# Kernel optimization log

Measured on AMD Instinct MI355X. Metric: run time of the kernel, lower is better.

## Reference

```python
import jax, jax.numpy as jnp
import numpy as np

B, N_COLS, N_PROMPTS, D = 1024, 256, 128, 256


def _ln(x, g, b, eps=1e-5):
    m = jnp.mean(x, axis=-1, keepdims=True)
    v = jnp.mean(jnp.square(x - m), axis=-1, keepdims=True)
    return (x - m) * jax.lax.rsqrt(v + eps) * g + b


def setup_inputs() -> dict:
    key = jax.random.key(0)
    ks = jax.random.split(key, 10)
    d_rs = D ** -0.5
    return {
        "x": jax.random.normal(ks[0], (B, N_COLS), jnp.float32),
        "prev_cell_out": jax.random.normal(ks[1], (B, N_PROMPTS, D), jnp.float32),
        "feature_emb_weight": jax.random.uniform(ks[2], (N_COLS, D), jnp.float32, -d_rs, d_rs),
        "feature_emb_bias": jax.random.uniform(ks[3], (N_COLS, D), jnp.float32, -d_rs, d_rs),
        "ln_emb_g": jnp.ones((D,), jnp.float32),
        "ln_emb_b": jnp.zeros((D,), jnp.float32),
        "ln_col_g": jnp.ones((D,), jnp.float32),
        "ln_col_b": jnp.zeros((D,), jnp.float32),
        "ln_prompt_g": jnp.ones((D,), jnp.float32),
        "ln_prompt_b": jnp.zeros((D,), jnp.float32),
        # torch Linear(2*D, D): weight [D, 2*D], y = x @ W^T + b
        "dense_imp_w": jax.random.normal(ks[4], (D, 2 * D), jnp.float32) * (2 * D) ** -0.5,
        "dense_imp_b": jnp.zeros((D,), jnp.float32),
        "emb_column": jax.random.normal(ks[5], (N_COLS, D), jnp.float32) * 0.01,
        "emb_prompt": jax.random.normal(ks[6], (N_PROMPTS, D), jnp.float32) * 0.01,
        # dense_expand = Linear(1, n_prompts): weight [n_prompts,1] squeezed -> [n_prompts]
        "expand_w": jax.random.normal(ks[7], (N_PROMPTS,), jnp.float32),
        "expand_b": jax.random.normal(ks[8], (N_PROMPTS,), jnp.float32) * 0.01,
    }


def reference(x, prev_cell_out, feature_emb_weight, feature_emb_bias,
              ln_emb_g, ln_emb_b, ln_col_g, ln_col_b, ln_prompt_g, ln_prompt_b,
              dense_imp_w, dense_imp_b, emb_column, emb_prompt,
              expand_w, expand_b):
    # feature embedding: [B, N, D]
    x_emb = jax.nn.relu(jnp.einsum('bn,nd->bnd', x, feature_emb_weight) + feature_emb_bias)
    x_emb = _ln(x_emb, ln_emb_g, ln_emb_b)
    # prompt update with residual
    xp = jnp.broadcast_to(emb_prompt[None], (x.shape[0], N_PROMPTS, D))  # [B, P, D]
    cat = jnp.concatenate([_ln(xp, ln_prompt_g, ln_prompt_b), prev_cell_out], axis=-1)  # [B, P, 2D]
    xp = jnp.einsum('bpk,dk->bpd', cat, dense_imp_w) + dense_imp_b + xp
    # column keys (shared across batch)
    col = _ln(emb_column, ln_col_g, ln_col_b)  # [N, D]
    mask = jax.nn.softmax(jnp.einsum('bpd,nd->bpn', xp, col), axis=-1)  # [B, P, N]
    V = jnp.einsum('bpn,bnd->bpd', mask, x_emb)  # [B, P, D]
    return V * (1.0 + expand_w)[None, :, None] + expand_b[None, :, None]
```

## Files before the change

kernel.cpp:

```cpp
#include <hip/hip_runtime.h>

#define NCOLS 256
#define NP    128
#define DD    256

typedef _Float16 half2 __attribute__((ext_vector_type(2)));
typedef _Float16 half4 __attribute__((ext_vector_type(4)));
typedef _Float16 half8 __attribute__((ext_vector_type(8)));
typedef float    f32x4 __attribute__((ext_vector_type(4)));

#define MFMA16(a,b,c) __builtin_amdgcn_mfma_f32_16x16x16f16(a,b,c,0,0,0)
#define MFMA32(a,b,c) __builtin_amdgcn_mfma_f32_16x16x32_f16(a,b,c,0,0,0)

#define WS_COL_LN   0
#define WS_BASE     393216
#define WS_BLOG     524288
#define WS_CW16     655360
#define WS_WB16     786432

#define LDS_CWP   3072
#define LDS_XE0   68608
#define LDS_XE1   101376
#define SMEM_MAIN 134144

__global__ __launch_bounds__(256) void k_prep1(
    const float* __restrict__ emb_column, const float* __restrict__ emb_prompt,
    const float* __restrict__ ln_col_g, const float* __restrict__ ln_col_b,
    const float* __restrict__ ln_prompt_g, const float* __restrict__ ln_prompt_b,
    const float* __restrict__ few, const float* __restrict__ feb,
    const float* __restrict__ diw, const float* __restrict__ dib,
    char* __restrict__ ws)
{
    __shared__ float red[10];
    __shared__ float rowv[DD];
    int blk = blockIdx.x, tid = threadIdx.x;

    if (blk < 384) {
        bool isCol = blk < 256;
        int r = isCol ? blk : blk - 256;
        const float* src = (isCol ? emb_column : emb_prompt) + r*DD;
        const float* g   = isCol ? ln_col_g : ln_prompt_g;
        const float* bb  = isCol ? ln_col_b : ln_prompt_b;

        float v = src[tid];
        float s = v, q = v*v;
        #pragma unroll
        for (int off = 32; off; off >>= 1) { s += __shfl_xor(s, off); q += __shfl_xor(q, off); }
        int wid = tid >> 6, lane = tid & 63;
        if (lane == 0) { red[wid] = s; red[4+wid] = q; }
        __syncthreads();
        if (tid == 0) {
            float S = red[0]+red[1]+red[2]+red[3];
            float Q = red[4]+red[5]+red[6]+red[7];
            float mu = S * (1.0f/DD);
            float var = Q * (1.0f/DD) - mu*mu;
            red[8] = mu; red[9] = rsqrtf(var + 1e-5f);
        }
        __syncthreads();
        float ln = (v - red[8]) * red[9] * g[tid] + bb[tid];
        rowv[tid] = ln;
        if (isCol) ((float*)(ws + WS_COL_LN))[r*DD + tid] = ln;
        __syncthreads();

        if (isCol) {
            int n = r;
            float acc = 0.f;
            #pragma unroll 4
            for (int d = 0; d < DD; ++d) acc += rowv[d] * diw[d*512 + 256 + tid];
            int nt = n >> 4, lr = n & 15;
            int kc32 = tid >> 5, lq = (tid >> 3) & 3, jj = tid & 7;
            ((_Float16*)(ws + WS_CW16))[(kc32*16 + nt)*512 + (lq*16 + lr)*8 + jj] = (_Float16)acc;
        } else {
            int p = r;
            float acc = 0.f;
            #pragma unroll 4
            for (int k = 0; k < DD; ++k) acc += rowv[k] * diw[tid*512 + k];
            ((float*)(ws + WS_BASE))[p*DD + tid] = acc + dib[tid] + emb_prompt[p*DD + tid];
        }
    } else {
        int base = (blk - 384) * 512;
        half2* wb = (half2*)(ws + WS_WB16);
        #pragma unroll
        for (int j = 0; j < 2; ++j) {
            int idx = base + j*256 + tid;
            half2 h; h[0] = (_Float16)few[idx]; h[1] = (_Float16)feb[idx];
            wb[idx] = h;
        }
    }
}

__global__ __launch_bounds__(256) void k_prep2(char* __restrict__ ws)
{
    __shared__ float bs[DD];
    int p = blockIdx.x, n = threadIdx.x;
    const float* base   = (const float*)(ws + WS_BASE);
    const float* col_ln = (const float*)(ws + WS_COL_LN);
    bs[n] = base[p*DD + n];
    __syncthreads();
    float acc = 0.f;
    #pragma unroll 4
    for (int d = 0; d < DD; ++d) acc += bs[d] * col_ln[n*DD + d];
    ((float*)(ws + WS_BLOG))[p*DD + n] = acc;
}

__global__ __launch_bounds__(1024) void trompt_main(
    const float* __restrict__ x, const float* __restrict__ prev,
    const float* __restrict__ expand_w, const float* __restrict__ expand_b,
    const float* __restrict__ ln_emb_g, const float* __restrict__ ln_emb_b,
    const char* __restrict__ ws, float* __restrict__ out)
{
    extern __shared__ char smem[];
    float* x_s  = (float*)(smem);
    float* sm_m = (float*)(smem + 1024);
    float* sm_l = (float*)(smem + 2048);
    char*  cwP  = smem + LDS_CWP;
    char*  xe0  = smem + LDS_XE0;
    char*  xe1  = smem + LDS_XE1;

    const char*  cwbase = ws + WS_CW16;
    const half2* WB     = (const half2*)(ws + WS_WB16);

    int b = blockIdx.x;
    int tid = threadIdx.x;
    int w = tid >> 6, l = tid & 63, lq = l >> 4, lr = l & 15;
    int pt = w >> 1, h = w & 1;
    int p  = 16*pt + lr;
    int pswz = (p & 7) << 4;

    if (tid < 256) x_s[tid] = x[b*NCOLS + tid];

    half8 pf[8];
    {
        const float* prow = prev + ((size_t)b*NP + p)*DD + 8*lq;
        #pragma unroll
        for (int kc = 0; kc < 8; ++kc) {
            f32x4 v0 = *(const f32x4*)(prow + 32*kc);
            f32x4 v1 = *(const f32x4*)(prow + 32*kc + 4);
            half8 hh;
            #pragma unroll
            for (int j = 0; j < 4; ++j) { hh[j] = (_Float16)v0[j]; hh[4+j] = (_Float16)v1[j]; }
            pf[kc] = hh;
        }
    }

    f32x4 acc[8];
    {
        const float* blrow = (const float*)(ws + WS_BLOG) + (size_t)p*DD + 4*lq;
        #pragma unroll
        for (int a = 0; a < 8; ++a) acc[a] = *(const f32x4*)(blrow + 16*(8*h + a));
    }

    #pragma unroll
    for (int i = 0; i < 8; ++i) {
        int u = tid + 1024*i;
        *(uint4*)(cwP + u*16) = *(const uint4*)(cwbase + u*16);
    }

    __syncthreads();

    {
        const char* cwl = cwP + (size_t)(8*h)*1024 + l*16;
        #pragma unroll
        for (int kc = 0; kc < 8; ++kc) {
            const char* fb = cwl + (size_t)kc*16384;
            half8 bp = pf[kc];
            #pragma unroll
            for (int a = 0; a < 8; ++a)
                acc[a] = MFMA32(*(const half8*)(fb + a*1024), bp, acc[a]);
        }
    }

    float mh = -1e30f;
    #pragma unroll
    for (int a = 0; a < 8; ++a)
        #pragma unroll
        for (int r = 0; r < 4; ++r) mh = fmaxf(mh, acc[a][r]);
    mh = fmaxf(mh, __shfl_xor(mh, 16));
    mh = fmaxf(mh, __shfl_xor(mh, 32));

    float sh = 0.f;
    #pragma unroll
    for (int a = 0; a < 8; ++a)
        #pragma unroll
        for (int r = 0; r < 4; ++r) { float e = __expf(acc[a][r] - mh); acc[a][r] = e; sh += e; }
    sh += __shfl_xor(sh, 16);
    sh += __shfl_xor(sh, 32);

    if (lq == 0) { sm_m[h*128 + p] = mh; sm_l[h*128 + p] = sh; }
    __syncthreads();
    float mo = sm_m[(1 ^ h)*128 + p];
    float so = sm_l[(1 ^ h)*128 + p];
    float M  = fmaxf(mh, mo);
    float eh = __expf(mh - M), eo = __expf(mo - M);
    float fac = eh / (sh*eh + so*eo);

    #pragma unroll
    for (int a = 0; a < 8; ++a) {
        int nb = (8*h + a)*32 + lq*8;
        half4 hh;
        #pragma unroll
        for (int r = 0; r < 4; ++r) hh[r] = (_Float16)(acc[a][r] * fac);
        *(half4*)(cwP + p*512 + (nb ^ pswz)) = hh;
    }

    float gcc[4], bcc[4];
    #pragma unroll
    for (int cc = 0; cc < 4; ++cc) {
        gcc[cc] = ln_emb_g[l + 64*cc];
        bcc[cc] = ln_emb_b[l + 64*cc];
    }

    int kc2w = w >> 2, lq2 = w & 3;
    auto compute_xe = [&](int c, char* xebuf) {
        float vj[4][4];
        #pragma unroll
        for (int j = 0; j < 4; ++j) {
            int n = c*64 + 16*kc2w + 4*lq2 + j;
            float xv = x_s[n];
            const half2* wbrow = WB + n*DD;
            float ss = 0.f, qq = 0.f;
            #pragma unroll
            for (int cc = 0; cc < 4; ++cc) {
                half2 pp = wbrow[l + 64*cc];
                float e = fmaf(xv, (float)pp[0], (float)pp[1]);
                e = e > 0.f ? e : 0.f;
                vj[j][cc] = e; ss += e; qq += e*e;
            }
            #pragma unroll
            for (int off = 32; off; off >>= 1) { ss += __shfl_xor(ss, off); qq += __shfl_xor(qq, off); }
            float mu = ss * (1.0f/DD);
            float rs = rsqrtf(qq*(1.0f/DD) - mu*mu + 1e-5f);
            #pragma unroll
            for (int cc = 0; cc < 4; ++cc)
                vj[j][cc] = (vj[j][cc]-mu)*rs*gcc[cc] + bcc[cc];
        }
        #pragma unroll
        for (int cc = 0; cc < 4; ++cc) {
            int dt = 4*cc + (l >> 4);
            half4 hh;
            #pragma unroll
            for (int j = 0; j < 4; ++j) hh[j] = (_Float16)vj[j][cc];
            *(half4*)(xebuf + (((kc2w*16 + dt)*64) + lq2*16 + lr)*8) = hh;
        }
    };

    compute_xe(0, xe0);

    f32x4 acc_v[8];
    #pragma unroll
    for (int dtl = 0; dtl < 8; ++dtl) acc_v[dtl] = (f32x4){0.f,0.f,0.f,0.f};

    __syncthreads();

    for (int c = 0; c < 4; ++c) {
        char* xec = (c & 1) ? xe1 : xe0;
        char* xen = (c & 1) ? xe0 : xe1;

        half4 bp[4];
        #pragma unroll
        for (int kc2 = 0; kc2 < 4; ++kc2)
            bp[kc2] = *(const half4*)(cwP + p*512 + ((c*128 + kc2*32 + lq*8) ^ pswz));

        if (c < 3) compute_xe(c+1, xen);

        const char* xel = xec + l*8;
        #pragma unroll
        for (int kc2 = 0; kc2 < 4; ++kc2) {
            const char* xb = xel + (size_t)(kc2*16 + 8*h)*512;
            half4 bpc = bp[kc2];
            #pragma unroll
            for (int dtl = 0; dtl < 8; ++dtl)
                acc_v[dtl] = MFMA16(*(const half4*)(xb + dtl*512), bpc, acc_v[dtl]);
        }

        if (c < 3) __syncthreads();
    }

    {
        float sw = 1.0f + expand_w[p];
        float sb = expand_b[p];
        float* orow = out + ((size_t)b*NP + p)*DD + 128*h + 4*lq;
        #pragma unroll
        for (int dtl = 0; dtl < 8; ++dtl) {
            f32x4 v = acc_v[dtl];
            #pragma unroll
            for (int r = 0; r < 4; ++r) v[r] = v[r]*sw + sb;
            *(f32x4*)(orow + 16*dtl) = v;
        }
    }
}

extern "C" void kernel_launch(void* const* d_in, const int* in_sizes, int n_in,
                              void* d_out, int out_size, void* d_ws, size_t ws_size,
                              hipStream_t stream) {
    (void)in_sizes; (void)n_in; (void)out_size; (void)ws_size;
    const float* x           = (const float*)d_in[0];
    const float* prev        = (const float*)d_in[1];
    const float* few         = (const float*)d_in[2];
    const float* feb         = (const float*)d_in[3];
    const float* ln_emb_g    = (const float*)d_in[4];
    const float* ln_emb_b    = (const float*)d_in[5];
    const float* ln_col_g    = (const float*)d_in[6];
    const float* ln_col_b    = (const float*)d_in[7];
    const float* ln_prompt_g = (const float*)d_in[8];
    const float* ln_prompt_b = (const float*)d_in[9];
    const float* diw         = (const float*)d_in[10];
    const float* dib         = (const float*)d_in[11];
    const float* emb_column  = (const float*)d_in[12];
    const float* emb_prompt  = (const float*)d_in[13];
    const float* expand_w    = (const float*)d_in[14];
    const float* expand_b    = (const float*)d_in[15];
    char* ws = (char*)d_ws;
    float* out = (float*)d_out;

    k_prep1<<<512, 256, 0, stream>>>(emb_column, emb_prompt, ln_col_g, ln_col_b,
                                     ln_prompt_g, ln_prompt_b, few, feb,
                                     diw, dib, ws);
    k_prep2<<<128, 256, 0, stream>>>(ws);

    (void)hipFuncSetAttribute(reinterpret_cast<const void*>(trompt_main),
                              hipFuncAttributeMaxDynamicSharedMemorySize, SMEM_MAIN);
    trompt_main<<<1024, 1024, SMEM_MAIN, stream>>>(x, prev, expand_w, expand_b,
                                                   ln_emb_g, ln_emb_b, ws, out);
}
```

Before: 181.3 us.

## Make main kernel persistent over four batches with prefetch of next batch inputs

The main kernel now launches 256 blocks, and each block loops over four batch rows instead of handling one. While the softmax and value stages of the current row run, it prefetches the next row's prev_cell_out fragment into registers and its x row into a second LDS buffer. The aim is to hide global load latency and amortise block launch and setup, since the LN gains and bias pointers are loaded once per block. In exchange there is less parallelism (256 blocks on a 256-CU part), more live registers from holding the prefetched fragment, and the column-weight tile is reloaded into LDS every iteration because its space is reused for the mask.

```diff
diff --git a/kernel.cpp b/kernel.cpp
--- a/kernel.cpp
+++ b/kernel.cpp
@@ -18,10 +18,10 @@
 #define WS_CW16     655360
 #define WS_WB16     786432
 
-#define LDS_CWP   3072
-#define LDS_XE0   68608
-#define LDS_XE1   101376
-#define SMEM_MAIN 134144
+#define LDS_CWP   4096
+#define LDS_XE0   69632
+#define LDS_XE1   102400
+#define SMEM_MAIN 135168
 
 __global__ __launch_bounds__(256) void k_prep1(
     const float* __restrict__ emb_column, const float* __restrict__ emb_prompt,
@@ -110,9 +110,10 @@
     const char* __restrict__ ws, float* __restrict__ out)
 {
     extern __shared__ char smem[];
-    float* x_s  = (float*)(smem);
-    float* sm_m = (float*)(smem + 1024);
-    float* sm_l = (float*)(smem + 2048);
+    float* x_sA = (float*)(smem);
+    float* x_sB = (float*)(smem + 1024);
+    float* sm_m = (float*)(smem + 2048);
+    float* sm_l = (float*)(smem + 3072);
     char*  cwP  = smem + LDS_CWP;
     char*  xe0  = smem + LDS_XE0;
     char*  xe1  = smem + LDS_XE1;
@@ -120,88 +121,13 @@
     const char*  cwbase = ws + WS_CW16;
     const half2* WB     = (const half2*)(ws + WS_WB16);
 
-    int b = blockIdx.x;
+    int bid = blockIdx.x;
     int tid = threadIdx.x;
     int w = tid >> 6, l = tid & 63, lq = l >> 4, lr = l & 15;
     int pt = w >> 1, h = w & 1;
     int p  = 16*pt + lr;
     int pswz = (p & 7) << 4;
-
-    if (tid < 256) x_s[tid] = x[b*NCOLS + tid];
-
-    half8 pf[8];
-    {
-        const float* prow = prev + ((size_t)b*NP + p)*DD + 8*lq;
-        #pragma unroll
-        for (int kc = 0; kc < 8; ++kc) {
-            f32x4 v0 = *(const f32x4*)(prow + 32*kc);
-            f32x4 v1 = *(const f32x4*)(prow + 32*kc + 4);
-            half8 hh;
-            #pragma unroll
-            for (int j = 0; j < 4; ++j) { hh[j] = (_Float16)v0[j]; hh[4+j] = (_Float16)v1[j]; }
-            pf[kc] = hh;
-        }
-    }
-
-    f32x4 acc[8];
-    {
-        const float* blrow = (const float*)(ws + WS_BLOG) + (size_t)p*DD + 4*lq;
-        #pragma unroll
-        for (int a = 0; a < 8; ++a) acc[a] = *(const f32x4*)(blrow + 16*(8*h + a));
-    }
-
-    #pragma unroll
-    for (int i = 0; i < 8; ++i) {
-        int u = tid + 1024*i;
-        *(uint4*)(cwP + u*16) = *(const uint4*)(cwbase + u*16);
-    }
-
-    __syncthreads();
-
-    {
-        const char* cwl = cwP + (size_t)(8*h)*1024 + l*16;
-        #pragma unroll
-        for (int kc = 0; kc < 8; ++kc) {
-            const char* fb = cwl + (size_t)kc*16384;
-            half8 bp = pf[kc];
-            #pragma unroll
-            for (int a = 0; a < 8; ++a)
-                acc[a] = MFMA32(*(const half8*)(fb + a*1024), bp, acc[a]);
-        }
-    }
-
-    float mh = -1e30f;
-    #pragma unroll
-    for (int a = 0; a < 8; ++a)
-        #pragma unroll
-        for (int r = 0; r < 4; ++r) mh = fmaxf(mh, acc[a][r]);
-    mh = fmaxf(mh, __shfl_xor(mh, 16));
-    mh = fmaxf(mh, __shfl_xor(mh, 32));
-
-    float sh = 0.f;
-    #pragma unroll
-    for (int a = 0; a < 8; ++a)
-        #pragma unroll
-        for (int r = 0; r < 4; ++r) { float e = __expf(acc[a][r] - mh); acc[a][r] = e; sh += e; }
-    sh += __shfl_xor(sh, 16);
-    sh += __shfl_xor(sh, 32);
-
-    if (lq == 0) { sm_m[h*128 + p] = mh; sm_l[h*128 + p] = sh; }
-    __syncthreads();
-    float mo = sm_m[(1 ^ h)*128 + p];
-    float so = sm_l[(1 ^ h)*128 + p];
-    float M  = fmaxf(mh, mo);
-    float eh = __expf(mh - M), eo = __expf(mo - M);
-    float fac = eh / (sh*eh + so*eo);
-
-    #pragma unroll
-    for (int a = 0; a < 8; ++a) {
-        int nb = (8*h + a)*32 + lq*8;
-        half4 hh;
-        #pragma unroll
-        for (int r = 0; r < 4; ++r) hh[r] = (_Float16)(acc[a][r] * fac);
-        *(half4*)(cwP + p*512 + (nb ^ pswz)) = hh;
-    }
+    int kc2w = w >> 2, lq2 = w & 3;
 
     float gcc[4], bcc[4];
     #pragma unroll
@@ -209,14 +135,28 @@
         gcc[cc] = ln_emb_g[l + 64*cc];
         bcc[cc] = ln_emb_b[l + 64*cc];
     }
-
-    int kc2w = w >> 2, lq2 = w & 3;
-    auto compute_xe = [&](int c, char* xebuf) {
+    const float* blrow = (const float*)(ws + WS_BLOG) + (size_t)p*DD + 4*lq;
+
+    half8 pf[8];
+    auto load_pf = [&](int bb) {
+        const float* prow = prev + ((size_t)bb*NP + p)*DD + 8*lq;
+        #pragma unroll
+        for (int kc = 0; kc < 8; ++kc) {
+            f32x4 v0 = *(const f32x4*)(prow + 32*kc);
+            f32x4 v1 = *(const f32x4*)(prow + 32*kc + 4);
+            half8 hh;
+            #pragma unroll
+            for (int j = 0; j < 4; ++j) { hh[j] = (_Float16)v0[j]; hh[4+j] = (_Float16)v1[j]; }
+            pf[kc] = hh;
+        }
+    };
+
+    auto compute_xe = [&](const float* xs, int c, char* xebuf) {
         float vj[4][4];
         #pragma unroll
         for (int j = 0; j < 4; ++j) {
             int n = c*64 + 16*kc2w + 4*lq2 + j;
-            float xv = x_s[n];
+            float xv = xs[n];
             const half2* wbrow = WB + n*DD;
             float ss = 0.f, qq = 0.f;
             #pragma unroll
@@ -244,48 +184,122 @@
         }
     };
 
-    compute_xe(0, xe0);
-
-    f32x4 acc_v[8];
-    #pragma unroll
-    for (int dtl = 0; dtl < 8; ++dtl) acc_v[dtl] = (f32x4){0.f,0.f,0.f,0.f};
-
-    __syncthreads();
-
-    for (int c = 0; c < 4; ++c) {
-        char* xec = (c & 1) ? xe1 : xe0;
-        char* xen = (c & 1) ? xe0 : xe1;
-
-        half4 bp[4];
-        #pragma unroll
-        for (int kc2 = 0; kc2 < 4; ++kc2)
-            bp[kc2] = *(const half4*)(cwP + p*512 + ((c*128 + kc2*32 + lq*8) ^ pswz));
-
-        if (c < 3) compute_xe(c+1, xen);
-
-        const char* xel = xec + l*8;
-        #pragma unroll
-        for (int kc2 = 0; kc2 < 4; ++kc2) {
-            const char* xb = xel + (size_t)(kc2*16 + 8*h)*512;
-            half4 bpc = bp[kc2];
-            #pragma unroll
-            for (int dtl = 0; dtl < 8; ++dtl)
-                acc_v[dtl] = MFMA16(*(const half4*)(xb + dtl*512), bpc, acc_v[dtl]);
-        }
-
-        if (c < 3) __syncthreads();
-    }
-
-    {
-        float sw = 1.0f + expand_w[p];
-        float sb = expand_b[p];
-        float* orow = out + ((size_t)b*NP + p)*DD + 128*h + 4*lq;
-        #pragma unroll
-        for (int dtl = 0; dtl < 8; ++dtl) {
-            f32x4 v = acc_v[dtl];
-            #pragma unroll
-            for (int r = 0; r < 4; ++r) v[r] = v[r]*sw + sb;
-            *(f32x4*)(orow + 16*dtl) = v;
+    if (tid < 256) x_sA[tid] = x[bid*NCOLS + tid];
+    load_pf(bid);
+
+    #pragma unroll 1
+    for (int it = 0; it < 4; ++it) {
+        int b = bid + 256*it;
+        const float* xs  = (it & 1) ? x_sB : x_sA;
+        float*       xsn = (it & 1) ? x_sA : x_sB;
+
+        __syncthreads();
+
+        #pragma unroll
+        for (int i = 0; i < 8; ++i) {
+            int u = tid + 1024*i;
+            *(uint4*)(cwP + u*16) = *(const uint4*)(cwbase + u*16);
+        }
+
+        f32x4 acc[8];
+        #pragma unroll
+        for (int a = 0; a < 8; ++a) acc[a] = *(const f32x4*)(blrow + 16*(8*h + a));
+
+        __syncthreads();
+
+        {
+            const char* cwl = cwP + (size_t)(8*h)*1024 + l*16;
+            #pragma unroll
+            for (int kc = 0; kc < 8; ++kc) {
+                const char* fb = cwl + (size_t)kc*16384;
+                half8 bp = pf[kc];
+                #pragma unroll
+                for (int a = 0; a < 8; ++a)
+                    acc[a] = MFMA32(*(const half8*)(fb + a*1024), bp, acc[a]);
+            }
+        }
+
+        if (it < 3) {
+            load_pf(b + 256);
+            if (tid < 256) xsn[tid] = x[(b + 256)*NCOLS + tid];
+        }
+
+        float mh = -1e30f;
+        #pragma unroll
+        for (int a = 0; a < 8; ++a)
+            #pragma unroll
+            for (int r = 0; r < 4; ++r) mh = fmaxf(mh, acc[a][r]);
+        mh = fmaxf(mh, __shfl_xor(mh, 16));
+        mh = fmaxf(mh, __shfl_xor(mh, 32));
+
+        float sh = 0.f;
+        #pragma unroll
+        for (int a = 0; a < 8; ++a)
+            #pragma unroll
+            for (int r = 0; r < 4; ++r) { float e = __expf(acc[a][r] - mh); acc[a][r] = e; sh += e; }
+        sh += __shfl_xor(sh, 16);
+        sh += __shfl_xor(sh, 32);
+
+        if (lq == 0) { sm_m[h*128 + p] = mh; sm_l[h*128 + p] = sh; }
+        __syncthreads();
+        float mo = sm_m[(1 ^ h)*128 + p];
+        float so = sm_l[(1 ^ h)*128 + p];
+        float M  = fmaxf(mh, mo);
+        float eh = __expf(mh - M), eo = __expf(mo - M);
+        float fac = eh / (sh*eh + so*eo);
+
+        #pragma unroll
+        for (int a = 0; a < 8; ++a) {
+            int nb = (8*h + a)*32 + lq*8;
+            half4 hh;
+            #pragma unroll
+            for (int r = 0; r < 4; ++r) hh[r] = (_Float16)(acc[a][r] * fac);
+            *(half4*)(cwP + p*512 + (nb ^ pswz)) = hh;
+        }
+
+        compute_xe(xs, 0, xe0);
+
+        f32x4 acc_v[8];
+        #pragma unroll
+        for (int dtl = 0; dtl < 8; ++dtl) acc_v[dtl] = (f32x4){0.f,0.f,0.f,0.f};
+
+        __syncthreads();
+
+        for (int c = 0; c < 4; ++c) {
+            char* xec = (c & 1) ? xe1 : xe0;
+            char* xen = (c & 1) ? xe0 : xe1;
+
+            half4 bp[4];
+            #pragma unroll
+            for (int kc2 = 0; kc2 < 4; ++kc2)
+                bp[kc2] = *(const half4*)(cwP + p*512 + ((c*128 + kc2*32 + lq*8) ^ pswz));
+
+            if (c < 3) compute_xe(xs, c+1, xen);
+
+            const char* xel = xec + l*8;
+            #pragma unroll
+            for (int kc2 = 0; kc2 < 4; ++kc2) {
+                const char* xb = xel + (size_t)(kc2*16 + 8*h)*512;
+                half4 bpc = bp[kc2];
+                #pragma unroll
+                for (int dtl = 0; dtl < 8; ++dtl)
+                    acc_v[dtl] = MFMA16(*(const half4*)(xb + dtl*512), bpc, acc_v[dtl]);
+            }
+
+            if (c < 3) __syncthreads();
+        }
+
+        {
+            float sw = 1.0f + expand_w[p];
+            float sb = expand_b[p];
+            float* orow = out + ((size_t)b*NP + p)*DD + 128*h + 4*lq;
+            #pragma unroll
+            for (int dtl = 0; dtl < 8; ++dtl) {
+                f32x4 v = acc_v[dtl];
+                #pragma unroll
+                for (int r = 0; r < 4; ++r) v[r] = v[r]*sw + sb;
+                *(f32x4*)(orow + 16*dtl) = v;
+            }
         }
     }
 }
@@ -320,6 +334,6 @@
 
     (void)hipFuncSetAttribute(reinterpret_cast<const void*>(trompt_main),
                               hipFuncAttributeMaxDynamicSharedMemorySize, SMEM_MAIN);
-    trompt_main<<<1024, 1024, SMEM_MAIN, stream>>>(x, prev, expand_w, expand_b,
-                                                   ln_emb_g, ln_emb_b, ws, out);
+    trompt_main<<<256, 1024, SMEM_MAIN, stream>>>(x, prev, expand_w, expand_b,
+                                                  ln_emb_g, ln_emb_b, ws, out);
 }
```

Measured after the change: 314.6 us. 73.5% more time.
